# Kernel tuning notes

Hardware: AMD Instinct MI355X
Metric: run time of the kernel (lower is better)

The kernel has to match this reference:

```python
import jax, jax.numpy as jnp
import numpy as np
import math

B, C, P, D, H = 8, 128, 96, 128, 8
R = D // H          # per-head rank = 16
G = 512             # ff_dim (topic nodes)
LN_EPS = 1e-5
L1_EPS = 1e-6


def setup_inputs() -> dict:
    key = jax.random.key(0)
    ks = jax.random.split(key, 10)
    W = 0.02  # factor init scale (matches torch.randn(...)*0.02)
    return {
        "qz": jax.random.normal(ks[0], (B, C, P, D), jnp.float32),
        "unary": jax.random.normal(ks[1], (B, C, P, D), jnp.float32),
        "time_u": jax.random.normal(ks[2], (B, D, D), jnp.float32) * W,
        "time_v": jax.random.normal(ks[3], (B, D, D), jnp.float32) * W,
        "channel_u": jax.random.normal(ks[4], (B, D, D), jnp.float32) * W,
        "channel_v": jax.random.normal(ks[5], (B, D, D), jnp.float32) * W,
        "topic_binary": jax.random.normal(ks[6], (B, G, D), jnp.float32) * W,
        "ln_g": jnp.ones((D,), jnp.float32),
        "ln_b": jnp.zeros((D,), jnp.float32),
        "w1": jax.random.normal(ks[7], (D, D), jnp.float32) * (1.0 / math.sqrt(D)),
        "b1": jnp.zeros((D,), jnp.float32),
        "w2": jax.random.normal(ks[8], (D, D), jnp.float32) * (1.0 / math.sqrt(D)),
        "b2": jnp.zeros((D,), jnp.float32),
    }


def _layernorm(x, g, b):
    mu = x.mean(-1, keepdims=True)
    xc = x - mu
    var = (xc * xc).mean(-1, keepdims=True)
    return xc * jax.lax.rsqrt(var + LN_EPS) * g + b


def _heads(x, u_w):
    # per-batch projection: [B,C,P,D] x [B,O,D] -> [B,C,P,O] -> [B,C,P,H,R]
    return jnp.einsum('bcpd,bod->bcpo', x, u_w).reshape(B, C, P, H, R)


def _time_messages(qz, u_w, v_w):
    q_u = _heads(qz, u_w).transpose(0, 1, 3, 2, 4)  # bchpr
    q_v = _heads(qz, v_w).transpose(0, 1, 3, 2, 4)  # bchqr
    attn = jnp.einsum('bchpr,bchqr->bchpq', q_u, q_v) / math.sqrt(R)
    attn = jax.nn.softmax(attn, axis=-1)
    # einsum('bchpq,bcqd->bchpd') followed by mean over h == fused contraction / H
    return jnp.einsum('bchpq,bcqd->bcpd', attn, qz) / H


def _channel_messages(qz, u_w, v_w):
    q_u = _heads(qz, u_w).transpose(0, 2, 3, 1, 4)  # bphcr
    q_v = _heads(qz, v_w).transpose(0, 2, 3, 1, 4)  # bphdr
    attn = jnp.einsum('bphcr,bphdr->bphcd', q_u, q_v) / math.sqrt(R)
    attn = jax.nn.softmax(attn, axis=-1)            # [B,P,H,C,C]
    qz_patch = qz.transpose(0, 2, 1, 3)             # [B,P,C,D]  (requires C == D)
    # elementwise einsum('bphcd,bpcd->bphcd') then mean over h == mean_h(attn) * qz_patch
    msg = attn.mean(axis=2) * qz_patch              # [B,P,C,D]
    return msg.transpose(0, 2, 1, 3)                # [B,C,P,D]


def _topic_messages(qz, binary):
    qg = jax.nn.relu(jnp.einsum('bcpd,bgd->bcpg', qz, binary))
    qg = qg / jnp.maximum(qg.sum(-1, keepdims=True), L1_EPS)  # F.normalize(p=1)
    return jnp.einsum('bcpg,bgd->bcpd', qg, binary)


def reference(qz, unary, time_u, time_v, channel_u, channel_v, topic_binary,
              ln_g, ln_b, w1, b1, w2, b2):
    old = qz
    qz_n = _layernorm(qz, ln_g, ln_b)
    m_t = _time_messages(qz_n, time_u, time_v)
    m_c = _channel_messages(qz_n, channel_u, channel_v)
    m_g = _topic_messages(qz_n, topic_binary)
    qz = unary + m_t + m_c + m_g
    qz = 0.5 * (qz + old)
    h = _layernorm(qz, ln_g, ln_b)
    h = jax.nn.gelu(jnp.einsum('bcpd,od->bcpo', h, w1) + b1, approximate=False)
    h = jnp.einsum('bcpd,od->bcpo', h, w2) + b2
    return qz + h
```

## Files before the change

kernel.cpp:

```cpp
#include <hip/hip_runtime.h>
#include <math.h>

#define TB 8
#define TC 128
#define TP 96
#define TD 128
#define TH 8
#define TG 512

#define DOT4(va, vb) ((va).x*(vb).x + (va).y*(vb).y + (va).z*(vb).z + (va).w*(vb).w)

typedef __attribute__((ext_vector_type(8))) short  bf16x8_t;
typedef __attribute__((ext_vector_type(8))) unsigned short u16x8_t;
typedef __attribute__((ext_vector_type(4))) float  f32x4_t;

__device__ __forceinline__ unsigned short f2bf(float f) {
  unsigned u = __float_as_uint(f);
  unsigned r = (u + 0x7fffu + ((u >> 16) & 1u)) >> 16;
  return (unsigned short)r;
}
__device__ __forceinline__ float bf2f(unsigned short h) {
  return __uint_as_float((unsigned)h << 16);
}

template <int NROWS>
__device__ __forceinline__ void ln_rows(float (*src)[132], float (*dst)[132],
                                        int tid, const float* lng, const float* lnb)
{
  if (tid < NROWS * 4) {
    int r = tid >> 2, sub = tid & 3;
    float s = 0.f, s2 = 0.f;
    #pragma unroll
    for (int j = 0; j < 32; ++j) {
      float x = src[r][sub * 32 + j];
      s += x; s2 += x * x;
    }
    s  += __shfl_xor(s, 1);  s  += __shfl_xor(s, 2);
    s2 += __shfl_xor(s2, 1); s2 += __shfl_xor(s2, 2);
    float mu = s * (1.f / 128.f);
    float rs = rsqrtf(s2 * (1.f / 128.f) - mu * mu + 1e-5f);
    #pragma unroll
    for (int j = 0; j < 32; ++j) {
      int d = sub * 32 + j;
      dst[r][d] = (src[r][d] - mu) * rs * lng[d] + lnb[d];
    }
  }
}

__global__ __launch_bounds__(256) void k_prep(
    const float* __restrict__ bin, unsigned short* __restrict__ binB,
    unsigned short* __restrict__ binT)
{
  __shared__ unsigned short tile[64][132];
  const int tid = threadIdx.x;
  const int b = blockIdx.x >> 3;
  const int g0 = (blockIdx.x & 7) * 64;
  const size_t bb = (size_t)b * (TG * TD);

  #pragma unroll
  for (int i = 0; i < 8; ++i) {
    int idx4 = tid + i * 256;
    int g = idx4 >> 5;
    int d0 = (idx4 & 31) << 2;
    float4 v = *(const float4*)(bin + bb + (size_t)(g0 + g) * TD + d0);
    ushort4 h;
    h.x = f2bf(v.x); h.y = f2bf(v.y); h.z = f2bf(v.z); h.w = f2bf(v.w);
    *(ushort4*)(binB + bb + (size_t)(g0 + g) * TD + d0) = h;
    tile[g][d0] = h.x; tile[g][d0+1] = h.y; tile[g][d0+2] = h.z; tile[g][d0+3] = h.w;
  }
  __syncthreads();
  const int d = tid >> 1, half = tid & 1;
  unsigned short* dst = binT + (size_t)b * (TD * TG) + (size_t)d * TG + g0 + half * 32;
  #pragma unroll
  for (int i = 0; i < 8; ++i) {
    ushort4 o;
    o.x = tile[half*32 + 4*i + 0][d];
    o.y = tile[half*32 + 4*i + 1][d];
    o.z = tile[half*32 + 4*i + 2][d];
    o.w = tile[half*32 + 4*i + 3][d];
    *(ushort4*)(dst + 4*i) = o;
  }
}

__global__ __launch_bounds__(256) void k_prepw(
    const float* __restrict__ tu, const float* __restrict__ tv,
    const float* __restrict__ cu, const float* __restrict__ cv,
    unsigned short* __restrict__ wTu, unsigned short* __restrict__ wTv,
    unsigned short* __restrict__ wCu, unsigned short* __restrict__ wCv)
{
  const int m = blockIdx.x >> 7;
  const int off = (blockIdx.x & 127) * 1024 + threadIdx.x * 4;
  const float* src = (m == 0) ? tu : (m == 1) ? tv : (m == 2) ? cu : cv;
  unsigned short* dst = (m == 0) ? wTu : (m == 1) ? wTv : (m == 2) ? wCu : wCv;
  float4 v = *(const float4*)(src + off);
  ushort4 h;
  h.x = f2bf(v.x); h.y = f2bf(v.y); h.z = f2bf(v.z); h.w = f2bf(v.w);
  *(ushort4*)(dst + off) = h;
}

__global__ __launch_bounds__(384) void k_time(
    const float* __restrict__ qz, const unsigned short* __restrict__ wTu,
    const unsigned short* __restrict__ wTv, const float* __restrict__ lng,
    const float* __restrict__ lnb, float* __restrict__ out)
{
  __shared__ unsigned short zn [96][136];
  __shared__ unsigned short znT[128][104];
  __shared__ unsigned short qu [96][136];
  __shared__ unsigned short qv [96][136];

  const int tid = threadIdx.x;
  const int b = blockIdx.x >> 7;
  const int c = blockIdx.x & 127;
  const size_t base = (size_t)(b * TC + c) * (TP * TD);

  {
    const int r = tid >> 2, sub = tid & 3;
    float x[32];
    float s = 0.f, s2 = 0.f;
    #pragma unroll
    for (int i = 0; i < 8; ++i) {
      float4 v = *(const float4*)(qz + base + (size_t)r * TD + sub * 32 + i * 4);
      x[i*4+0] = v.x; x[i*4+1] = v.y; x[i*4+2] = v.z; x[i*4+3] = v.w;
      s += v.x + v.y + v.z + v.w;
      s2 += v.x*v.x + v.y*v.y + v.z*v.z + v.w*v.w;
    }
    s  += __shfl_xor(s, 1);  s  += __shfl_xor(s, 2);
    s2 += __shfl_xor(s2, 1); s2 += __shfl_xor(s2, 2);
    float mu = s * (1.f / 128.f);
    float rs = rsqrtf(s2 * (1.f / 128.f) - mu * mu + 1e-5f);
    unsigned short hv[32];
    #pragma unroll
    for (int j = 0; j < 32; ++j) {
      int d = sub * 32 + j;
      hv[j] = f2bf((x[j] - mu) * rs * lng[d] + lnb[d]);
    }
    #pragma unroll
    for (int j0 = 0; j0 < 32; j0 += 8) {
      u16x8_t v;
      #pragma unroll
      for (int j = 0; j < 8; ++j) v[j] = hv[j0 + j];
      *(u16x8_t*)&zn[r][sub * 32 + j0] = v;
    }
    #pragma unroll
    for (int j = 0; j < 32; ++j) znT[sub * 32 + j][r] = hv[j];
  }
  __syncthreads();

  const int l = tid & 63, w = tid >> 6;
  const int ln16 = l & 15, lg16 = l >> 4;
  const int prow = w * 16 + ln16;

  {
    bf16x8_t A[4];
    #pragma unroll
    for (int k = 0; k < 4; ++k)
      A[k] = *(const bf16x8_t*)&zn[prow][k*32 + lg16*8];
    #pragma unroll
    for (int m = 0; m < 2; ++m) {
      const unsigned short* W = ((m == 0) ? wTu : wTv) + (size_t)b * 16384;
      #pragma unroll
      for (int ot = 0; ot < 8; ++ot) {
        bf16x8_t Bf[4];
        #pragma unroll
        for (int k = 0; k < 4; ++k)
          Bf[k] = *(const bf16x8_t*)(W + (size_t)(ot*16 + ln16) * 128 + k*32 + lg16*8);
        f32x4_t acc = (f32x4_t)0.f;
        #pragma unroll
        for (int k = 0; k < 4; ++k)
          acc = __builtin_amdgcn_mfma_f32_16x16x32_bf16(A[k], Bf[k], acc, 0, 0, 0);
        unsigned short (*dst)[136] = (m == 0) ? qu : qv;
        #pragma unroll
        for (int rg = 0; rg < 4; ++rg)
          dst[w*16 + lg16*4 + rg][ot*16 + ln16] = f2bf(acc[rg]);
      }
    }
  }
  __syncthreads();

  f32x4_t asumT[6];
  #pragma unroll
  for (int et = 0; et < 6; ++et) asumT[et] = (f32x4_t)0.f;
  const bf16x8_t zfrag = (bf16x8_t)(short)0;
  const int koff = (lg16 & 1) * 8;
  for (int h = 0; h < TH; ++h) {
    bf16x8_t Bq = *(const bf16x8_t*)&qu[prow][h*16 + koff];
    if (lg16 >= 2) Bq = zfrag;
    f32x4_t T[6];
    #pragma unroll
    for (int et = 0; et < 6; ++et) {
      bf16x8_t Aq = *(const bf16x8_t*)&qv[et*16 + ln16][h*16 + koff];
      if (lg16 >= 2) Aq = zfrag;
      T[et] = __builtin_amdgcn_mfma_f32_16x16x32_bf16(Aq, Bq, (f32x4_t)0.f, 0, 0, 0);
    }
    float mx = -1e30f;
    #pragma unroll
    for (int et = 0; et < 6; ++et)
      #pragma unroll
      for (int rg = 0; rg < 4; ++rg) {
        T[et][rg] *= 0.25f;
        mx = fmaxf(mx, T[et][rg]);
      }
    mx = fmaxf(mx, __shfl_xor(mx, 16));
    mx = fmaxf(mx, __shfl_xor(mx, 32));
    float tot = 0.f;
    #pragma unroll
    for (int et = 0; et < 6; ++et)
      #pragma unroll
      for (int rg = 0; rg < 4; ++rg) {
        float e = __expf(T[et][rg] - mx);
        T[et][rg] = e; tot += e;
      }
    tot += __shfl_xor(tot, 16);
    tot += __shfl_xor(tot, 32);
    float inv = 1.f / tot;
    #pragma unroll
    for (int et = 0; et < 6; ++et)
      #pragma unroll
      for (int rg = 0; rg < 4; ++rg)
        asumT[et][rg] += T[et][rg] * inv;
  }
  __syncthreads();

  unsigned short (*asum)[104] = (unsigned short (*)[104])&qu[0][0];
  #pragma unroll
  for (int et = 0; et < 6; ++et) {
    ushort4 hv;
    hv.x = f2bf(asumT[et][0]); hv.y = f2bf(asumT[et][1]);
    hv.z = f2bf(asumT[et][2]); hv.w = f2bf(asumT[et][3]);
    *(ushort4*)&asum[w*16 + ln16][et*16 + lg16*4] = hv;
  }
  __syncthreads();

  {
    bf16x8_t Aa[3];
    #pragma unroll
    for (int k = 0; k < 3; ++k)
      Aa[k] = *(const bf16x8_t*)&asum[prow][k*32 + lg16*8];
    #pragma unroll
    for (int dt = 0; dt < 8; ++dt) {
      f32x4_t acc = (f32x4_t)0.f;
      #pragma unroll
      for (int k = 0; k < 3; ++k) {
        bf16x8_t Bz = *(const bf16x8_t*)&znT[dt*16 + ln16][k*32 + lg16*8];
        acc = __builtin_amdgcn_mfma_f32_16x16x32_bf16(Aa[k], Bz, acc, 0, 0, 0);
      }
      #pragma unroll
      for (int rg = 0; rg < 4; ++rg)
        out[base + (size_t)(w*16 + lg16*4 + rg) * TD + dt*16 + ln16] = acc[rg] * 0.125f;
    }
  }
}

__global__ __launch_bounds__(512) void k_channel(
    const float* __restrict__ qz, const unsigned short* __restrict__ wCu,
    const unsigned short* __restrict__ wCv, const float* __restrict__ lng,
    const float* __restrict__ lnb, float* __restrict__ out)
{
  __shared__ unsigned short patch[128][136];
  __shared__ unsigned short qu  [128][136];
  __shared__ unsigned short qv  [128][136];

  const int tid = threadIdx.x;
  const int b = blockIdx.x / TP;
  const int p = blockIdx.x - b * TP;
  const size_t bbase = (size_t)b * (TC * TP * TD);

  {
    const int r = tid >> 2, sub = tid & 3;
    float x[32];
    float s = 0.f, s2 = 0.f;
    #pragma unroll
    for (int i = 0; i < 8; ++i) {
      float4 v = *(const float4*)(qz + bbase + ((size_t)r * TP + p) * TD + sub * 32 + i * 4);
      x[i*4+0] = v.x; x[i*4+1] = v.y; x[i*4+2] = v.z; x[i*4+3] = v.w;
      s += v.x + v.y + v.z + v.w;
      s2 += v.x*v.x + v.y*v.y + v.z*v.z + v.w*v.w;
    }
    s  += __shfl_xor(s, 1);  s  += __shfl_xor(s, 2);
    s2 += __shfl_xor(s2, 1); s2 += __shfl_xor(s2, 2);
    float mu = s * (1.f / 128.f);
    float rs = rsqrtf(s2 * (1.f / 128.f) - mu * mu + 1e-5f);
    #pragma unroll
    for (int j0 = 0; j0 < 32; j0 += 8) {
      u16x8_t v;
      #pragma unroll
      for (int j = 0; j < 8; ++j) {
        int d = sub * 32 + j0 + j;
        v[j] = f2bf((x[j0 + j] - mu) * rs * lng[d] + lnb[d]);
      }
      *(u16x8_t*)&patch[r][sub * 32 + j0] = v;
    }
  }
  __syncthreads();

  const int l = tid & 63, w = tid >> 6;
  const int ln16 = l & 15, lg16 = l >> 4;
  const int crow = w * 16 + ln16;

  {
    bf16x8_t A[4];
    #pragma unroll
    for (int k = 0; k < 4; ++k)
      A[k] = *(const bf16x8_t*)&patch[crow][k*32 + lg16*8];
    #pragma unroll
    for (int m = 0; m < 2; ++m) {
      const unsigned short* W = ((m == 0) ? wCu : wCv) + (size_t)b * 16384;
      #pragma unroll
      for (int ot = 0; ot < 8; ++ot) {
        bf16x8_t Bf[4];
        #pragma unroll
        for (int k = 0; k < 4; ++k)
          Bf[k] = *(const bf16x8_t*)(W + (size_t)(ot*16 + ln16) * 128 + k*32 + lg16*8);
        f32x4_t acc = (f32x4_t)0.f;
        #pragma unroll
        for (int k = 0; k < 4; ++k)
          acc = __builtin_amdgcn_mfma_f32_16x16x32_bf16(A[k], Bf[k], acc, 0, 0, 0);
        unsigned short (*dst)[136] = (m == 0) ? qu : qv;
        #pragma unroll
        for (int rg = 0; rg < 4; ++rg)
          dst[w*16 + lg16*4 + rg][ot*16 + ln16] = f2bf(acc[rg]);
      }
    }
  }
  __syncthreads();

  f32x4_t asumT[8];
  #pragma unroll
  for (int et = 0; et < 8; ++et) asumT[et] = (f32x4_t)0.f;
  const bf16x8_t zfrag = (bf16x8_t)(short)0;
  const int koff = (lg16 & 1) * 8;
  for (int h = 0; h < TH; ++h) {
    bf16x8_t Bq = *(const bf16x8_t*)&qu[crow][h*16 + koff];
    if (lg16 >= 2) Bq = zfrag;
    f32x4_t T[8];
    #pragma unroll
    for (int et = 0; et < 8; ++et) {
      bf16x8_t Aq = *(const bf16x8_t*)&qv[et*16 + ln16][h*16 + koff];
      if (lg16 >= 2) Aq = zfrag;
      T[et] = __builtin_amdgcn_mfma_f32_16x16x32_bf16(Aq, Bq, (f32x4_t)0.f, 0, 0, 0);
    }
    float mx = -1e30f;
    #pragma unroll
    for (int et = 0; et < 8; ++et)
      #pragma unroll
      for (int rg = 0; rg < 4; ++rg) {
        T[et][rg] *= 0.25f;
        mx = fmaxf(mx, T[et][rg]);
      }
    mx = fmaxf(mx, __shfl_xor(mx, 16));
    mx = fmaxf(mx, __shfl_xor(mx, 32));
    float tot = 0.f;
    #pragma unroll
    for (int et = 0; et < 8; ++et)
      #pragma unroll
      for (int rg = 0; rg < 4; ++rg) {
        float e = __expf(T[et][rg] - mx);
        T[et][rg] = e; tot += e;
      }
    tot += __shfl_xor(tot, 16);
    tot += __shfl_xor(tot, 32);
    float inv = 1.f / tot;
    #pragma unroll
    for (int et = 0; et < 8; ++et)
      #pragma unroll
      for (int rg = 0; rg < 4; ++rg)
        asumT[et][rg] += T[et][rg] * inv;
  }

  {
    float* oa = out + bbase + ((size_t)crow * TP + p) * TD;
    #pragma unroll
    for (int et = 0; et < 8; ++et) {
      int f0 = et*16 + lg16*4;
      ushort4 ph = *(const ushort4*)&patch[crow][f0];
      float4 o4 = *(float4*)(oa + f0);
      o4.x += asumT[et][0] * 0.125f * bf2f(ph.x);
      o4.y += asumT[et][1] * 0.125f * bf2f(ph.y);
      o4.z += asumT[et][2] * 0.125f * bf2f(ph.z);
      o4.w += asumT[et][3] * 0.125f * bf2f(ph.w);
      *(float4*)(oa + f0) = o4;
    }
  }
}

__global__ __launch_bounds__(512) void k_topic(
    const float* __restrict__ qz, const unsigned short* __restrict__ binB,
    const unsigned short* __restrict__ binT, const float* __restrict__ lng,
    const float* __restrict__ lnb, float* __restrict__ out)
{
  __shared__ unsigned short zn [128][136];
  __shared__ unsigned short bt [128][136];
  __shared__ unsigned short btT[128][136];
  __shared__ unsigned short qg [128][136];
  __shared__ float rsum[4][128];

  const int tid = threadIdx.x;
  const int b = blockIdx.x / 96;
  const size_t row0 = (size_t)blockIdx.x * 128;
  const unsigned short* binBb = binB + (size_t)b * (TG * TD);
  const unsigned short* binTb = binT + (size_t)b * (TD * TG);

  {
    const int r = tid >> 2, sub = tid & 3;
    float x[32];
    float s = 0.f, s2 = 0.f;
    #pragma unroll
    for (int i = 0; i < 8; ++i) {
      float4 v = *(const float4*)(qz + (row0 + r) * TD + sub * 32 + i * 4);
      x[i*4+0] = v.x; x[i*4+1] = v.y; x[i*4+2] = v.z; x[i*4+3] = v.w;
      s += v.x + v.y + v.z + v.w;
      s2 += v.x*v.x + v.y*v.y + v.z*v.z + v.w*v.w;
    }
    s  += __shfl_xor(s, 1);  s  += __shfl_xor(s, 2);
    s2 += __shfl_xor(s2, 1); s2 += __shfl_xor(s2, 2);
    float mu = s * (1.f / 128.f);
    float rs = rsqrtf(s2 * (1.f / 128.f) - mu * mu + 1e-5f);
    #pragma unroll
    for (int j0 = 0; j0 < 32; j0 += 8) {
      u16x8_t v;
      #pragma unroll
      for (int j = 0; j < 8; ++j) {
        int d = sub * 32 + j0 + j;
        v[j] = f2bf((x[j0+j] - mu) * rs * lng[d] + lnb[d]);
      }
      *(u16x8_t*)&zn[r][sub * 32 + j0] = v;
    }
  }

  const int l = tid & 63;
  const int w = tid >> 6;
  const int wr = w >> 2;
  const int wc = w & 3;
  const int ln16 = l & 15, lg16 = l >> 4;

  f32x4_t macc[4][2];
  #pragma unroll
  for (int mi = 0; mi < 4; ++mi)
    #pragma unroll
    for (int ni = 0; ni < 2; ++ni) macc[mi][ni] = (f32x4_t)0.f;
  float rs_acc[4][4];
  #pragma unroll
  for (int mi = 0; mi < 4; ++mi)
    #pragma unroll
    for (int rg = 0; rg < 4; ++rg) rs_acc[mi][rg] = 0.f;

  for (int gt = 0; gt < 4; ++gt) {
    if (gt) __syncthreads();
    {
      const int row = tid >> 2, seg = tid & 3;
      const unsigned short* gsrc = binBb + (size_t)(gt * 128 + row) * TD + seg * 32;
      #pragma unroll
      for (int i = 0; i < 4; ++i)
        *(u16x8_t*)&bt[row][seg * 32 + i * 8] = *(const u16x8_t*)(gsrc + i * 8);
      const unsigned short* tsrc = binTb + (size_t)row * TG + gt * 128 + seg * 32;
      #pragma unroll
      for (int i = 0; i < 4; ++i)
        *(u16x8_t*)&btT[row][seg * 32 + i * 8] = *(const u16x8_t*)(tsrc + i * 8);
    }
    __syncthreads();

    {
      bf16x8_t B1[2][4];
      #pragma unroll
      for (int ni = 0; ni < 2; ++ni)
        #pragma unroll
        for (int k = 0; k < 4; ++k)
          B1[ni][k] = *(const bf16x8_t*)&bt[wc*32 + ni*16 + ln16][k*32 + lg16*8];
      #pragma unroll
      for (int mi = 0; mi < 4; ++mi) {
        const int r0 = wr*64 + mi*16;
        bf16x8_t A[4];
        #pragma unroll
        for (int k = 0; k < 4; ++k)
          A[k] = *(const bf16x8_t*)&zn[r0 + ln16][k*32 + lg16*8];
        #pragma unroll
        for (int ni = 0; ni < 2; ++ni) {
          f32x4_t acc = (f32x4_t)0.f;
          #pragma unroll
          for (int k = 0; k < 4; ++k)
            acc = __builtin_amdgcn_mfma_f32_16x16x32_bf16(A[k], B1[ni][k], acc, 0, 0, 0);
          #pragma unroll
          for (int rg = 0; rg < 4; ++rg) {
            float v = fmaxf(acc[rg], 0.f);
            rs_acc[mi][rg] += v;
            qg[r0 + lg16*4 + rg][wc*32 + ni*16 + ln16] = f2bf(v);
          }
        }
      }
    }
    __syncthreads();

    {
      bf16x8_t B2[2][4];
      #pragma unroll
      for (int ni = 0; ni < 2; ++ni)
        #pragma unroll
        for (int k = 0; k < 4; ++k)
          B2[ni][k] = *(const bf16x8_t*)&btT[wc*32 + ni*16 + ln16][k*32 + lg16*8];
      #pragma unroll
      for (int mi = 0; mi < 4; ++mi) {
        const int r0 = wr*64 + mi*16;
        bf16x8_t A2[4];
        #pragma unroll
        for (int k = 0; k < 4; ++k)
          A2[k] = *(const bf16x8_t*)&qg[r0 + ln16][k*32 + lg16*8];
        #pragma unroll
        for (int ni = 0; ni < 2; ++ni)
          #pragma unroll
          for (int k = 0; k < 4; ++k)
            macc[mi][ni] = __builtin_amdgcn_mfma_f32_16x16x32_bf16(A2[k], B2[ni][k], macc[mi][ni], 0, 0, 0);
      }
    }
  }

  #pragma unroll
  for (int mi = 0; mi < 4; ++mi)
    #pragma unroll
    for (int rg = 0; rg < 4; ++rg) {
      float s = rs_acc[mi][rg];
      s += __shfl_xor(s, 1); s += __shfl_xor(s, 2);
      s += __shfl_xor(s, 4); s += __shfl_xor(s, 8);
      rs_acc[mi][rg] = s;
    }
  if (ln16 == 0) {
    #pragma unroll
    for (int mi = 0; mi < 4; ++mi)
      #pragma unroll
      for (int rg = 0; rg < 4; ++rg)
        rsum[wc][wr*64 + mi*16 + lg16*4 + rg] = rs_acc[mi][rg];
  }
  __syncthreads();

  #pragma unroll
  for (int mi = 0; mi < 4; ++mi) {
    #pragma unroll
    for (int rg = 0; rg < 4; ++rg) {
      const int r = wr*64 + mi*16 + lg16*4 + rg;
      float tot = rsum[0][r] + rsum[1][r] + rsum[2][r] + rsum[3][r];
      float inv = 1.f / fmaxf(tot, 1e-6f);
      #pragma unroll
      for (int ni = 0; ni < 2; ++ni) {
        int d = wc*32 + ni*16 + ln16;
        out[(row0 + r) * TD + d] += macc[mi][ni][rg] * inv;
      }
    }
  }
}

__global__ __launch_bounds__(256) void k_final(
    const float* __restrict__ qz, const float* __restrict__ unary,
    const float* __restrict__ lng, const float* __restrict__ lnb,
    const float* __restrict__ w1, const float* __restrict__ b1,
    const float* __restrict__ w2, const float* __restrict__ b2,
    float* __restrict__ out)
{
  __shared__ float zmid[64][132];
  __shared__ float hbuf[64][132];
  __shared__ float wbuf[128][132];

  const int tid = threadIdx.x;
  const size_t row0 = (size_t)blockIdx.x * 64;

  #pragma unroll
  for (int i = 0; i < 8; ++i) {
    int idx4 = tid + i * 256;
    int r = idx4 >> 5;
    int d0 = (idx4 & 31) << 2;
    size_t a = (row0 + r) * TD + d0;
    float4 u4 = *(const float4*)(unary + a);
    float4 q4 = *(const float4*)(qz + a);
    float4 m4 = *(const float4*)(out + a);
    float4 z;
    z.x = 0.5f * (u4.x + m4.x + q4.x);
    z.y = 0.5f * (u4.y + m4.y + q4.y);
    z.z = 0.5f * (u4.z + m4.z + q4.z);
    z.w = 0.5f * (u4.w + m4.w + q4.w);
    *(float4*)&zmid[r][d0] = z;
  }
  __syncthreads();
  ln_rows<64>(zmid, hbuf, tid, lng, lnb);
  #pragma unroll
  for (int i = 0; i < 16; ++i) {
    int idx4 = tid + i * 256;
    int o = idx4 >> 5;
    int d0 = (idx4 & 31) << 2;
    *(float4*)&wbuf[o][d0] = *(const float4*)(w1 + (size_t)o * TD + d0);
  }
  __syncthreads();

  const int og = tid & 31, rg = tid >> 5;
  const int r0 = rg * 8;
  float acc[8][4];
  #pragma unroll
  for (int i = 0; i < 8; ++i)
    #pragma unroll
    for (int j = 0; j < 4; ++j) acc[i][j] = 0.f;
  for (int d4 = 0; d4 < TD; d4 += 4) {
    float4 a[8];
    #pragma unroll
    for (int i = 0; i < 8; ++i) a[i] = *(const float4*)&hbuf[r0 + i][d4];
    #pragma unroll
    for (int j = 0; j < 4; ++j) {
      float4 w = *(const float4*)&wbuf[og + 32 * j][d4];
      #pragma unroll
      for (int i = 0; i < 8; ++i) acc[i][j] += DOT4(a[i], w);
    }
  }
  float gel[8][4];
  #pragma unroll
  for (int j = 0; j < 4; ++j) {
    float bj = b1[og + 32 * j];
    #pragma unroll
    for (int i = 0; i < 8; ++i) {
      float x = acc[i][j] + bj;
      gel[i][j] = 0.5f * x * (1.f + erff(x * 0.70710678118654752f));
    }
  }
  __syncthreads();
  #pragma unroll
  for (int i = 0; i < 8; ++i)
    #pragma unroll
    for (int j = 0; j < 4; ++j) hbuf[r0 + i][og + 32 * j] = gel[i][j];
  #pragma unroll
  for (int i = 0; i < 16; ++i) {
    int idx4 = tid + i * 256;
    int o = idx4 >> 5;
    int d0 = (idx4 & 31) << 2;
    *(float4*)&wbuf[o][d0] = *(const float4*)(w2 + (size_t)o * TD + d0);
  }
  __syncthreads();

  float acc2[8][4];
  #pragma unroll
  for (int i = 0; i < 8; ++i)
    #pragma unroll
    for (int j = 0; j < 4; ++j) acc2[i][j] = 0.f;
  for (int d4 = 0; d4 < TD; d4 += 4) {
    float4 a[8];
    #pragma unroll
    for (int i = 0; i < 8; ++i) a[i] = *(const float4*)&hbuf[r0 + i][d4];
    #pragma unroll
    for (int j = 0; j < 4; ++j) {
      float4 w = *(const float4*)&wbuf[og + 32 * j][d4];
      #pragma unroll
      for (int i = 0; i < 8; ++i) acc2[i][j] += DOT4(a[i], w);
    }
  }
  #pragma unroll
  for (int j = 0; j < 4; ++j) {
    int o = og + 32 * j;
    float bj = b2[o];
    #pragma unroll
    for (int i = 0; i < 8; ++i) {
      out[(row0 + r0 + i) * TD + o] = zmid[r0 + i][o] + acc2[i][j] + bj;
    }
  }
}

extern "C" void kernel_launch(void* const* d_in, const int* in_sizes, int n_in,
                              void* d_out, int out_size, void* d_ws, size_t ws_size,
                              hipStream_t stream) {
  (void)in_sizes; (void)n_in; (void)out_size; (void)ws_size;
  const float* qz      = (const float*)d_in[0];
  const float* unary   = (const float*)d_in[1];
  const float* time_u  = (const float*)d_in[2];
  const float* time_v  = (const float*)d_in[3];
  const float* chan_u  = (const float*)d_in[4];
  const float* chan_v  = (const float*)d_in[5];
  const float* topic   = (const float*)d_in[6];
  const float* ln_g    = (const float*)d_in[7];
  const float* ln_b    = (const float*)d_in[8];
  const float* w1      = (const float*)d_in[9];
  const float* b1      = (const float*)d_in[10];
  const float* w2      = (const float*)d_in[11];
  const float* b2      = (const float*)d_in[12];
  float* out = (float*)d_out;

  unsigned short* binB = (unsigned short*)d_ws;
  unsigned short* binT = binB + (size_t)524288;
  unsigned short* wTu  = binT + (size_t)524288;
  unsigned short* wTv  = wTu + (size_t)131072;
  unsigned short* wCu  = wTv + (size_t)131072;
  unsigned short* wCv  = wCu + (size_t)131072;

  k_prep   <<<dim3(64), dim3(256), 0, stream>>>(topic, binB, binT);
  k_prepw  <<<dim3(512), dim3(256), 0, stream>>>(time_u, time_v, chan_u, chan_v,
                                                 wTu, wTv, wCu, wCv);
  k_time   <<<dim3(TB * TC), dim3(384), 0, stream>>>(qz, wTu, wTv, ln_g, ln_b, out);
  k_channel<<<dim3(TB * TP), dim3(512), 0, stream>>>(qz, wCu, wCv, ln_g, ln_b, out);
  k_topic  <<<dim3(TB * 96), dim3(512), 0, stream>>>(qz, binB, binT, ln_g, ln_b, out);
  k_final  <<<dim3(1536), dim3(256), 0, stream>>>(qz, unary, ln_g, ln_b, w1, b1, w2, b2, out);
}
```

Before: 593.6 us.

## Use bf16 MFMA for the final FFN and fuse layernorm into the load

The final FFN kernel moves from fp32 scalar FMA dot products to bf16 MFMA 16x16x32. Weights w1 and w2 are now converted to bf16 in the prep kernel, and B fragments are read straight from global memory. The residual sum and layernorm are computed in registers as rows load, and blocks grow to 128 rows with 512 threads. This cuts FP32 ALU work and shared-memory weight staging, at the cost of bf16 precision in the MLP.

Result: faster. 480.0 us (-19.1%).

```diff
diff --git a/kernel.cpp b/kernel.cpp
--- a/kernel.cpp
+++ b/kernel.cpp
@@ -8,8 +8,6 @@
 #define TH 8
 #define TG 512
 
-#define DOT4(va, vb) ((va).x*(vb).x + (va).y*(vb).y + (va).z*(vb).z + (va).w*(vb).w)
-
 typedef __attribute__((ext_vector_type(8))) short  bf16x8_t;
 typedef __attribute__((ext_vector_type(8))) unsigned short u16x8_t;
 typedef __attribute__((ext_vector_type(4))) float  f32x4_t;
@@ -21,30 +19,6 @@
 }
 __device__ __forceinline__ float bf2f(unsigned short h) {
   return __uint_as_float((unsigned)h << 16);
-}
-
-template <int NROWS>
-__device__ __forceinline__ void ln_rows(float (*src)[132], float (*dst)[132],
-                                        int tid, const float* lng, const float* lnb)
-{
-  if (tid < NROWS * 4) {
-    int r = tid >> 2, sub = tid & 3;
-    float s = 0.f, s2 = 0.f;
-    #pragma unroll
-    for (int j = 0; j < 32; ++j) {
-      float x = src[r][sub * 32 + j];
-      s += x; s2 += x * x;
-    }
-    s  += __shfl_xor(s, 1);  s  += __shfl_xor(s, 2);
-    s2 += __shfl_xor(s2, 1); s2 += __shfl_xor(s2, 2);
-    float mu = s * (1.f / 128.f);
-    float rs = rsqrtf(s2 * (1.f / 128.f) - mu * mu + 1e-5f);
-    #pragma unroll
-    for (int j = 0; j < 32; ++j) {
-      int d = sub * 32 + j;
-      dst[r][d] = (src[r][d] - mu) * rs * lng[d] + lnb[d];
-    }
-  }
 }
 
 __global__ __launch_bounds__(256) void k_prep(
@@ -85,13 +59,25 @@
 __global__ __launch_bounds__(256) void k_prepw(
     const float* __restrict__ tu, const float* __restrict__ tv,
     const float* __restrict__ cu, const float* __restrict__ cv,
+    const float* __restrict__ w1, const float* __restrict__ w2,
     unsigned short* __restrict__ wTu, unsigned short* __restrict__ wTv,
-    unsigned short* __restrict__ wCu, unsigned short* __restrict__ wCv)
+    unsigned short* __restrict__ wCu, unsigned short* __restrict__ wCv,
+    unsigned short* __restrict__ wW1, unsigned short* __restrict__ wW2)
 {
-  const int m = blockIdx.x >> 7;
-  const int off = (blockIdx.x & 127) * 1024 + threadIdx.x * 4;
-  const float* src = (m == 0) ? tu : (m == 1) ? tv : (m == 2) ? cu : cv;
-  unsigned short* dst = (m == 0) ? wTu : (m == 1) ? wTv : (m == 2) ? wCu : wCv;
+  const int bid = blockIdx.x;
+  const float* src; unsigned short* dst; size_t off;
+  if (bid < 512) {
+    const int m = bid >> 7;
+    off = (size_t)(bid & 127) * 1024 + threadIdx.x * 4;
+    src = (m == 0) ? tu : (m == 1) ? tv : (m == 2) ? cu : cv;
+    dst = (m == 0) ? wTu : (m == 1) ? wTv : (m == 2) ? wCu : wCv;
+  } else {
+    const int t = bid - 512;
+    const int m = t >> 4;
+    off = (size_t)(t & 15) * 1024 + threadIdx.x * 4;
+    src = m ? w2 : w1;
+    dst = m ? wW2 : wW1;
+  }
   float4 v = *(const float4*)(src + off);
   ushort4 h;
   h.x = f2bf(v.x); h.y = f2bf(v.y); h.z = f2bf(v.z); h.w = f2bf(v.w);
@@ -547,112 +533,126 @@
   }
 }
 
-__global__ __launch_bounds__(256) void k_final(
+__global__ __launch_bounds__(512) void k_final(
     const float* __restrict__ qz, const float* __restrict__ unary,
     const float* __restrict__ lng, const float* __restrict__ lnb,
-    const float* __restrict__ w1, const float* __restrict__ b1,
-    const float* __restrict__ w2, const float* __restrict__ b2,
+    const unsigned short* __restrict__ w1, const float* __restrict__ b1,
+    const unsigned short* __restrict__ w2, const float* __restrict__ b2,
     float* __restrict__ out)
 {
-  __shared__ float zmid[64][132];
-  __shared__ float hbuf[64][132];
-  __shared__ float wbuf[128][132];
+  __shared__ float zmid[128][132];
+  __shared__ unsigned short hn[128][136];
+  __shared__ unsigned short h2[128][136];
 
   const int tid = threadIdx.x;
-  const size_t row0 = (size_t)blockIdx.x * 64;
-
-  #pragma unroll
-  for (int i = 0; i < 8; ++i) {
-    int idx4 = tid + i * 256;
-    int r = idx4 >> 5;
-    int d0 = (idx4 & 31) << 2;
-    size_t a = (row0 + r) * TD + d0;
-    float4 u4 = *(const float4*)(unary + a);
-    float4 q4 = *(const float4*)(qz + a);
-    float4 m4 = *(const float4*)(out + a);
-    float4 z;
-    z.x = 0.5f * (u4.x + m4.x + q4.x);
-    z.y = 0.5f * (u4.y + m4.y + q4.y);
-    z.z = 0.5f * (u4.z + m4.z + q4.z);
-    z.w = 0.5f * (u4.w + m4.w + q4.w);
-    *(float4*)&zmid[r][d0] = z;
-  }
-  __syncthreads();
-  ln_rows<64>(zmid, hbuf, tid, lng, lnb);
-  #pragma unroll
-  for (int i = 0; i < 16; ++i) {
-    int idx4 = tid + i * 256;
-    int o = idx4 >> 5;
-    int d0 = (idx4 & 31) << 2;
-    *(float4*)&wbuf[o][d0] = *(const float4*)(w1 + (size_t)o * TD + d0);
-  }
-  __syncthreads();
-
-  const int og = tid & 31, rg = tid >> 5;
-  const int r0 = rg * 8;
-  float acc[8][4];
-  #pragma unroll
-  for (int i = 0; i < 8; ++i)
-    #pragma unroll
-    for (int j = 0; j < 4; ++j) acc[i][j] = 0.f;
-  for (int d4 = 0; d4 < TD; d4 += 4) {
-    float4 a[8];
-    #pragma unroll
-    for (int i = 0; i < 8; ++i) a[i] = *(const float4*)&hbuf[r0 + i][d4];
-    #pragma unroll
-    for (int j = 0; j < 4; ++j) {
-      float4 w = *(const float4*)&wbuf[og + 32 * j][d4];
-      #pragma unroll
-      for (int i = 0; i < 8; ++i) acc[i][j] += DOT4(a[i], w);
-    }
-  }
-  float gel[8][4];
-  #pragma unroll
-  for (int j = 0; j < 4; ++j) {
-    float bj = b1[og + 32 * j];
+  const size_t row0 = (size_t)blockIdx.x * 128;
+
+  {
+    const int r = tid >> 2, sub = tid & 3;
+    const size_t rowa = (row0 + r) * TD + sub * 32;
+    float x[32];
+    float s = 0.f, s2 = 0.f;
     #pragma unroll
     for (int i = 0; i < 8; ++i) {
-      float x = acc[i][j] + bj;
-      gel[i][j] = 0.5f * x * (1.f + erff(x * 0.70710678118654752f));
-    }
-  }
-  __syncthreads();
-  #pragma unroll
-  for (int i = 0; i < 8; ++i)
-    #pragma unroll
-    for (int j = 0; j < 4; ++j) hbuf[r0 + i][og + 32 * j] = gel[i][j];
-  #pragma unroll
-  for (int i = 0; i < 16; ++i) {
-    int idx4 = tid + i * 256;
-    int o = idx4 >> 5;
-    int d0 = (idx4 & 31) << 2;
-    *(float4*)&wbuf[o][d0] = *(const float4*)(w2 + (size_t)o * TD + d0);
-  }
-  __syncthreads();
-
-  float acc2[8][4];
-  #pragma unroll
-  for (int i = 0; i < 8; ++i)
-    #pragma unroll
-    for (int j = 0; j < 4; ++j) acc2[i][j] = 0.f;
-  for (int d4 = 0; d4 < TD; d4 += 4) {
-    float4 a[8];
-    #pragma unroll
-    for (int i = 0; i < 8; ++i) a[i] = *(const float4*)&hbuf[r0 + i][d4];
-    #pragma unroll
-    for (int j = 0; j < 4; ++j) {
-      float4 w = *(const float4*)&wbuf[og + 32 * j][d4];
-      #pragma unroll
-      for (int i = 0; i < 8; ++i) acc2[i][j] += DOT4(a[i], w);
-    }
-  }
-  #pragma unroll
-  for (int j = 0; j < 4; ++j) {
-    int o = og + 32 * j;
-    float bj = b2[o];
-    #pragma unroll
-    for (int i = 0; i < 8; ++i) {
-      out[(row0 + r0 + i) * TD + o] = zmid[r0 + i][o] + acc2[i][j] + bj;
+      float4 q4 = *(const float4*)(qz + rowa + i * 4);
+      float4 u4 = *(const float4*)(unary + rowa + i * 4);
+      float4 m4 = *(const float4*)(out + rowa + i * 4);
+      float4 z;
+      z.x = 0.5f * (u4.x + m4.x + q4.x);
+      z.y = 0.5f * (u4.y + m4.y + q4.y);
+      z.z = 0.5f * (u4.z + m4.z + q4.z);
+      z.w = 0.5f * (u4.w + m4.w + q4.w);
+      *(float4*)&zmid[r][sub * 32 + i * 4] = z;
+      x[i*4+0] = z.x; x[i*4+1] = z.y; x[i*4+2] = z.z; x[i*4+3] = z.w;
+      s += z.x + z.y + z.z + z.w;
+      s2 += z.x*z.x + z.y*z.y + z.z*z.z + z.w*z.w;
+    }
+    s  += __shfl_xor(s, 1);  s  += __shfl_xor(s, 2);
+    s2 += __shfl_xor(s2, 1); s2 += __shfl_xor(s2, 2);
+    float mu = s * (1.f / 128.f);
+    float rs = rsqrtf(s2 * (1.f / 128.f) - mu * mu + 1e-5f);
+    #pragma unroll
+    for (int j0 = 0; j0 < 32; j0 += 8) {
+      u16x8_t v;
+      #pragma unroll
+      for (int j = 0; j < 8; ++j) {
+        int d = sub * 32 + j0 + j;
+        v[j] = f2bf((x[j0 + j] - mu) * rs * lng[d] + lnb[d]);
+      }
+      *(u16x8_t*)&hn[r][sub * 32 + j0] = v;
+    }
+  }
+  __syncthreads();
+
+  const int l = tid & 63, w = tid >> 6;
+  const int wr = w >> 2, wc = w & 3;
+  const int ln16 = l & 15, lg16 = l >> 4;
+  const int bcol = wc * 32 + ln16;
+
+  {
+    bf16x8_t Bf[2][4];
+    float b1v[2];
+    #pragma unroll
+    for (int ni = 0; ni < 2; ++ni) {
+      b1v[ni] = b1[bcol + ni * 16];
+      #pragma unroll
+      for (int k = 0; k < 4; ++k)
+        Bf[ni][k] = *(const bf16x8_t*)(w1 + (size_t)(bcol + ni * 16) * 128 + k*32 + lg16*8);
+    }
+    #pragma unroll
+    for (int mi = 0; mi < 4; ++mi) {
+      const int r0 = wr * 64 + mi * 16;
+      bf16x8_t A[4];
+      #pragma unroll
+      for (int k = 0; k < 4; ++k)
+        A[k] = *(const bf16x8_t*)&hn[r0 + ln16][k*32 + lg16*8];
+      #pragma unroll
+      for (int ni = 0; ni < 2; ++ni) {
+        f32x4_t acc = (f32x4_t)0.f;
+        #pragma unroll
+        for (int k = 0; k < 4; ++k)
+          acc = __builtin_amdgcn_mfma_f32_16x16x32_bf16(A[k], Bf[ni][k], acc, 0, 0, 0);
+        #pragma unroll
+        for (int rg = 0; rg < 4; ++rg) {
+          float xx = acc[rg] + b1v[ni];
+          float g = 0.5f * xx * (1.f + erff(xx * 0.70710678118654752f));
+          h2[r0 + lg16*4 + rg][bcol + ni * 16] = f2bf(g);
+        }
+      }
+    }
+  }
+  __syncthreads();
+
+  {
+    bf16x8_t Bf[2][4];
+    float b2v[2];
+    #pragma unroll
+    for (int ni = 0; ni < 2; ++ni) {
+      b2v[ni] = b2[bcol + ni * 16];
+      #pragma unroll
+      for (int k = 0; k < 4; ++k)
+        Bf[ni][k] = *(const bf16x8_t*)(w2 + (size_t)(bcol + ni * 16) * 128 + k*32 + lg16*8);
+    }
+    #pragma unroll
+    for (int mi = 0; mi < 4; ++mi) {
+      const int r0 = wr * 64 + mi * 16;
+      bf16x8_t A[4];
+      #pragma unroll
+      for (int k = 0; k < 4; ++k)
+        A[k] = *(const bf16x8_t*)&h2[r0 + ln16][k*32 + lg16*8];
+      #pragma unroll
+      for (int ni = 0; ni < 2; ++ni) {
+        f32x4_t acc = (f32x4_t)0.f;
+        #pragma unroll
+        for (int k = 0; k < 4; ++k)
+          acc = __builtin_amdgcn_mfma_f32_16x16x32_bf16(A[k], Bf[ni][k], acc, 0, 0, 0);
+        #pragma unroll
+        for (int rg = 0; rg < 4; ++rg) {
+          const int rr = r0 + lg16*4 + rg;
+          const int cc = bcol + ni * 16;
+          out[(row0 + rr) * TD + cc] = zmid[rr][cc] + acc[rg] + b2v[ni];
+        }
+      }
     }
   }
 }
@@ -682,12 +682,14 @@
   unsigned short* wTv  = wTu + (size_t)131072;
   unsigned short* wCu  = wTv + (size_t)131072;
   unsigned short* wCv  = wCu + (size_t)131072;
+  unsigned short* wW1  = wCv + (size_t)131072;
+  unsigned short* wW2  = wW1 + (size_t)16384;
 
   k_prep   <<<dim3(64), dim3(256), 0, stream>>>(topic, binB, binT);
-  k_prepw  <<<dim3(512), dim3(256), 0, stream>>>(time_u, time_v, chan_u, chan_v,
-                                                 wTu, wTv, wCu, wCv);
+  k_prepw  <<<dim3(544), dim3(256), 0, stream>>>(time_u, time_v, chan_u, chan_v, w1, w2,
+                                                 wTu, wTv, wCu, wCv, wW1, wW2);
   k_time   <<<dim3(TB * TC), dim3(384), 0, stream>>>(qz, wTu, wTv, ln_g, ln_b, out);
   k_channel<<<dim3(TB * TP), dim3(512), 0, stream>>>(qz, wCu, wCv, ln_g, ln_b, out);
   k_topic  <<<dim3(TB * 96), dim3(512), 0, stream>>>(qz, binB, binT, ln_g, ln_b, out);
-  k_final  <<<dim3(1536), dim3(256), 0, stream>>>(qz, unary, ln_g, ln_b, w1, b1, w2, b2, out);
-}
+  k_final  <<<dim3(768), dim3(512), 0, stream>>>(qz, unary, ln_g, ln_b, wW1, b1, wW2, b2, out);
+}
```
